# Optimization experiments

Hardware: AMD Instinct MI355X
Metric: run time of the kernel (lower is better)

The kernel has to match this reference:

```python
import jax, jax.numpy as jnp
import numpy as np

THETA = 10000.0

def apply_rope(x, positions):
    # x: [B, H, S, d_k], positions: [S] int
    d_k = x.shape[-1]
    inv_freq = THETA ** (-jnp.arange(0, d_k, 2, dtype=jnp.float32) / d_k)  # [d_k/2]
    ang = positions.astype(jnp.float32)[:, None] * inv_freq[None, :]        # [S, d_k/2]
    cos, sin = jnp.cos(ang), jnp.sin(ang)
    x_even = x[..., 0::2]
    x_odd = x[..., 1::2]
    r_even = x_even * cos - x_odd * sin
    r_odd = x_even * sin + x_odd * cos
    # interleave back
    return jnp.stack([r_even, r_odd], axis=-1).reshape(x.shape)

def setup_inputs() -> dict:
    key = jax.random.key(0)
    k1, k2, k3 = jax.random.split(key, 3)
    B, S, D = 2, 2048, 1024
    x = jax.random.normal(k1, (B, S, D), dtype=jnp.float32)
    token_positions = jnp.arange(S, dtype=jnp.int32)
    W_qkv = jax.random.normal(k2, (3 * D, D), dtype=jnp.float32) * 0.02
    W_o = jax.random.normal(k3, (D, D), dtype=jnp.float32) * 0.02
    return {"x": x, "token_positions": token_positions, "W_qkv": W_qkv, "W_o": W_o}

def reference(x, token_positions, W_qkv, W_o):
    B, S, D = x.shape
    H = 16
    d_k = D // H
    qkv = jnp.einsum('bsd,ed->bse', x, W_qkv)           # [B, S, 3D]
    q, k, v = jnp.split(qkv, 3, axis=-1)
    def to_heads(t):
        return t.reshape(B, S, H, d_k).transpose(0, 2, 1, 3)  # [B, H, S, d_k]
    hq, hk, hv = to_heads(q), to_heads(k), to_heads(v)
    hq = apply_rope(hq, token_positions)
    hk = apply_rope(hk, token_positions)
    scale = d_k ** -0.5
    scores = jnp.einsum('bhqd,bhkd->bhqk', hq, hk) * scale  # [B, H, S, S]
    causal = jnp.tril(jnp.ones((S, S), dtype=bool))
    scores = jnp.where(causal, scores, -jnp.inf)
    attn = jax.nn.softmax(scores, axis=-1)
    out = jnp.einsum('bhqk,bhkd->bhqd', attn, hv)           # [B, H, S, d_k]
    out = out.transpose(0, 2, 1, 3).reshape(B, S, D)
    return jnp.einsum('bsd,ed->bse', out, W_o)
```

## Files before the change

kernel.cpp:

```cpp
#include <hip/hip_runtime.h>
#include <math.h>

typedef short short8 __attribute__((ext_vector_type(8)));
typedef float f32x4 __attribute__((ext_vector_type(4)));
typedef unsigned int u32x2 __attribute__((ext_vector_type(2)));

typedef __attribute__((address_space(1))) const void* as1p;
typedef __attribute__((address_space(3))) void* as3p;

__device__ __forceinline__ unsigned short f2bf(float f) {
    unsigned int u = __float_as_uint(f);
    u += 0x7fffu + ((u >> 16) & 1u);
    return (unsigned short)(u >> 16);
}

__global__ void cvt_all_bf16(const float* __restrict__ x,
                             const float* __restrict__ wqkv,
                             const float* __restrict__ wo,
                             unsigned short* __restrict__ xb,
                             unsigned short* __restrict__ wqkvb,
                             unsigned short* __restrict__ wob) {
    int i = blockIdx.x * blockDim.x + threadIdx.x;
    const float* src;
    unsigned short* dst;
    int off;
    if (i < 1048576)       { src = x;    dst = xb;    off = i; }
    else if (i < 1835008)  { src = wqkv; dst = wqkvb; off = i - 1048576; }
    else                   { src = wo;   dst = wob;   off = i - 1835008; }
    float4 v = ((const float4*)src)[off];
    ushort4 o = make_ushort4(f2bf(v.x), f2bf(v.y), f2bf(v.z), f2bf(v.w));
    ((ushort4*)dst)[off] = o;
}

template <int RF, int NTX, bool BF16_OUT, bool DO_ROPE>
__global__ __launch_bounds__(256) void gemm_nt_mfma(
    const unsigned short* __restrict__ A, const unsigned short* __restrict__ B,
    void* __restrict__ Cv, const int* __restrict__ pos, int N, int K) {
    constexpr int BM = RF * 32;
    __shared__ unsigned short As[BM * 32];
    __shared__ unsigned short Bs[128 * 32];
    const int tid = threadIdx.x;
    const int wave = tid >> 6, lane = tid & 63;
    const int L = blockIdx.x;
    const int xcd = L & 7, idx = L >> 3;
    const int nt_ = xcd * NTX + idx % NTX;
    const int mt  = idx / NTX;
    const int m0 = mt * BM, n0 = nt_ << 7;
    const int wr = ((wave >> 1) & 1) * (RF * 16);
    const int wc = (wave & 1) << 6;

    const int r0 = tid >> 2;
    const int ko = (((tid & 3) ^ ((r0 >> 1) & 3)) << 3);
    const unsigned short* Ap0 = A + (size_t)(m0 + r0) * K + ko;
    const unsigned short* Ap1 = A + (size_t)(m0 + (RF == 4 ? 64 : 0) + r0) * K + ko;
    const unsigned short* Bp0 = B + (size_t)(n0 + r0) * K + ko;
    const unsigned short* Bp1 = B + (size_t)(n0 + 64 + r0) * K + ko;

    f32x4 acc[RF][4] = {};
    const int lro = lane & 15;
    const int cs = ((lane >> 4) ^ ((lro >> 1) & 3)) << 3;

    for (int k0 = 0; k0 < K; k0 += 32) {
        __syncthreads();
        __builtin_amdgcn_global_load_lds((as1p)(Ap0 + k0), (as3p)(As + tid * 8), 16, 0, 0);
        if constexpr (RF == 4)
            __builtin_amdgcn_global_load_lds((as1p)(Ap1 + k0), (as3p)(As + (256 + tid) * 8), 16, 0, 0);
        __builtin_amdgcn_global_load_lds((as1p)(Bp0 + k0), (as3p)(Bs + tid * 8), 16, 0, 0);
        __builtin_amdgcn_global_load_lds((as1p)(Bp1 + k0), (as3p)(Bs + (256 + tid) * 8), 16, 0, 0);
        __syncthreads();

        short8 af[RF], bfr[4];
        #pragma unroll
        for (int i = 0; i < RF; i++) af[i] = *(const short8*)&As[(wr + i * 16 + lro) * 32 + cs];
        #pragma unroll
        for (int j = 0; j < 4; j++) bfr[j] = *(const short8*)&Bs[(wc + j * 16 + lro) * 32 + cs];
        #pragma unroll
        for (int i = 0; i < RF; i++)
            #pragma unroll
            for (int j = 0; j < 4; j++)
                acc[i][j] = __builtin_amdgcn_mfma_f32_16x16x32_bf16(af[i], bfr[j], acc[i][j], 0, 0, 0);
    }

    const int row_b = m0 + wr + ((lane >> 4) << 2);
    const int col_b = n0 + wc + lro;

    if constexpr (DO_ROPE) {
        const int sec = (n0 + wc) >> 10;
        if (sec < 2) {
            const float qs = (sec == 0) ? 0.18033688011112042f : 1.0f;
            const float sgn = (lane & 1) ? 1.0f : -1.0f;
            float ps[RF * 4];
            #pragma unroll
            for (int i = 0; i < RF; i++)
                #pragma unroll
                for (int r = 0; r < 4; r++)
                    ps[i * 4 + r] = (float)pos[(row_b + i * 16 + r) & 2047];
            #pragma unroll
            for (int j = 0; j < 4; j++) {
                float invf_rev = exp2f(-(float)((lro >> 1) + 8 * j) * 0.41524101186092029f)
                                 * 0.15915494309189535f;
                #pragma unroll
                for (int i = 0; i < RF; i++)
                    #pragma unroll
                    for (int r = 0; r < 4; r++) {
                        float rev = ps[i * 4 + r] * invf_rev;
                        rev -= floorf(rev);
                        float c = __builtin_amdgcn_cosf(rev) * qs;
                        float s = __builtin_amdgcn_sinf(rev) * (qs * sgn);
                        float mine = acc[i][j][r];
                        float partner = __shfl_xor(mine, 1, 64);
                        acc[i][j][r] = mine * c + partner * s;
                    }
            }
        }
    }

    #pragma unroll
    for (int i = 0; i < RF; i++)
        #pragma unroll
        for (int j = 0; j < 4; j++)
            #pragma unroll
            for (int r = 0; r < 4; r++) {
                size_t idx2 = (size_t)(row_b + i * 16 + r) * N + (col_b + j * 16);
                if constexpr (BF16_OUT) ((unsigned short*)Cv)[idx2] = f2bf(acc[i][j][r]);
                else ((float*)Cv)[idx2] = acc[i][j][r];
            }
}

__global__ __launch_bounds__(256, 3) void flash_attn_mfma(
    const unsigned short* __restrict__ qkv, unsigned short* __restrict__ Ows) {
    const int S = 2048, D3 = 3072;
    const int L = blockIdx.x;
    const int xcd = L & 7, rr = L >> 3;
    const int qt = 31 - (rr >> 2);
    const int g2 = xcd + ((rr & 3) << 3);
    const int h = g2 & 15, b = g2 >> 4;
    const int tid = threadIdx.x, wave = tid >> 6, lane = tid & 63;
    const int lro = lane & 15, grp = lane >> 4;

    __shared__ __align__(16) unsigned int Vp[64 * 34];
    __shared__ float RedW[4][16][66];
    __shared__ float Lbuf[4][4][16];

    const int kp = lane >> 3;
    const int vo = (lane & 7) << 3;
    const int wcb = wave << 3;
    const int klb = (wave << 4) + (grp << 2);

    const unsigned short* kbg = qkv + (size_t)(b * S) * D3 + 1024 + h * 64;
    const unsigned short* vbg = qkv + (size_t)(b * S) * D3 + 2048 + h * 64;

    const int q0 = qt << 6;
    const int nkt = qt + 1;

    short8 bq[4][2];
    #pragma unroll
    for (int f = 0; f < 4; f++) {
        const unsigned short* qrow =
            qkv + (size_t)(b * S + q0 + f * 16 + lro) * D3 + h * 64 + grp * 8;
        bq[f][0] = *(const short8*)qrow;
        bq[f][1] = *(const short8*)(qrow + 32);
    }

    const unsigned short* kfp = kbg + (size_t)(16 * wave + lro) * D3 + grp * 8;
    const unsigned short* vfp = vbg + (size_t)(16 * wave + 2 * kp) * D3 + vo;

    short8 kc0 = *(const short8*)kfp;
    short8 kc1 = *(const short8*)(kfp + 32);
    {
        uint4 va = *(const uint4*)vfp;
        uint4 vb = *(const uint4*)(vfp + D3);
        const unsigned short* pa_ = (const unsigned short*)&va;
        const unsigned short* pb_ = (const unsigned short*)&vb;
        #pragma unroll
        for (int j = 0; j < 8; j++)
            Vp[(vo + j) * 34 + wcb + kp] = (unsigned)pa_[j] | ((unsigned)pb_[j] << 16);
    }

    f32x4 acc[4][4] = {};
    float lsum[4] = {0.f, 0.f, 0.f, 0.f};

    for (int kt = 0; kt < nkt; kt++) {
        const bool pf = (kt + 1 < nkt);
        short8 kn0, kn1;
        uint4 vna, vnb;
        if (pf) {
            const size_t off = (size_t)((kt + 1) * 64) * D3;
            kn0 = *(const short8*)(kfp + off);
            kn1 = *(const short8*)(kfp + off + 32);
            vna = *(const uint4*)(vfp + off);
            vnb = *(const uint4*)(vfp + off + D3);
        }

        f32x4 s0 = {}, s1 = {}, s2 = {}, s3 = {};
        s0 = __builtin_amdgcn_mfma_f32_16x16x32_bf16(kc0, bq[0][0], s0, 0, 0, 0);
        s0 = __builtin_amdgcn_mfma_f32_16x16x32_bf16(kc1, bq[0][1], s0, 0, 0, 0);
        s1 = __builtin_amdgcn_mfma_f32_16x16x32_bf16(kc0, bq[1][0], s1, 0, 0, 0);
        s1 = __builtin_amdgcn_mfma_f32_16x16x32_bf16(kc1, bq[1][1], s1, 0, 0, 0);
        s2 = __builtin_amdgcn_mfma_f32_16x16x32_bf16(kc0, bq[2][0], s2, 0, 0, 0);
        s2 = __builtin_amdgcn_mfma_f32_16x16x32_bf16(kc1, bq[2][1], s2, 0, 0, 0);
        s3 = __builtin_amdgcn_mfma_f32_16x16x32_bf16(kc0, bq[3][0], s3, 0, 0, 0);
        s3 = __builtin_amdgcn_mfma_f32_16x16x32_bf16(kc1, bq[3][1], s3, 0, 0, 0);
        f32x4 sf[4] = {s0, s1, s2, s3};

        const bool dg = (kt == nkt - 1);
        u32x2 pw[4];
        #pragma unroll
        for (int f = 0; f < 4; f++) {
            float v0 = sf[f][0], v1 = sf[f][1], v2 = sf[f][2], v3 = sf[f][3];
            if (dg) {
                int thr = (f << 4) + lro - klb;
                if (0 > thr) v0 = -1e30f;
                if (1 > thr) v1 = -1e30f;
                if (2 > thr) v2 = -1e30f;
                if (3 > thr) v3 = -1e30f;
            }
            float p0 = __builtin_amdgcn_exp2f(v0);
            float p1 = __builtin_amdgcn_exp2f(v1);
            float p2 = __builtin_amdgcn_exp2f(v2);
            float p3 = __builtin_amdgcn_exp2f(v3);
            lsum[f] += (p0 + p1) + (p2 + p3);
            unsigned u0, u1;
            asm("v_cvt_pk_bf16_f32 %0, %1, %2" : "=v"(u0) : "v"(p0), "v"(p1));
            asm("v_cvt_pk_bf16_f32 %0, %1, %2" : "=v"(u1) : "v"(p2), "v"(p3));
            pw[f][0] = u0;
            pw[f][1] = u1;
        }

        u32x2 vv[4];
        #pragma unroll
        for (int nt = 0; nt < 4; nt++)
            vv[nt] = *(const u32x2*)&Vp[(nt * 16 + lro) * 34 + wcb + (grp << 1)];

        #pragma unroll
        for (int f = 0; f < 4; f++)
            #pragma unroll
            for (int nt = 0; nt < 4; nt++)
                asm("v_mfma_f32_16x16x16_bf16 %0, %1, %2, %0"
                    : "+v"(acc[f][nt]) : "v"(pw[f]), "v"(vv[nt]));

        if (pf) {
            const unsigned short* pa_ = (const unsigned short*)&vna;
            const unsigned short* pb_ = (const unsigned short*)&vnb;
            #pragma unroll
            for (int j = 0; j < 8; j++)
                Vp[(vo + j) * 34 + wcb + kp] = (unsigned)pa_[j] | ((unsigned)pb_[j] << 16);
            kc0 = kn0;
            kc1 = kn1;
        }
    }

    #pragma unroll
    for (int f = 0; f < 4; f++) {
        lsum[f] += __shfl_xor(lsum[f], 16, 64);
        lsum[f] += __shfl_xor(lsum[f], 32, 64);
    }
    if (lane < 16) {
        #pragma unroll
        for (int f = 0; f < 4; f++) Lbuf[wave][f][lro] = lsum[f];
    }

    #pragma unroll
    for (int f = 0; f < 4; f++) {
        __syncthreads();
        if (wave != f) {
            #pragma unroll
            for (int nt = 0; nt < 4; nt++)
                #pragma unroll
                for (int r = 0; r < 4; r++)
                    RedW[wave][(grp << 2) + r][nt * 16 + lro] = acc[f][nt][r];
        }
        __syncthreads();
        if (wave == f) {
            #pragma unroll
            for (int w2 = 0; w2 < 4; w2++) {
                if (w2 == f) continue;
                #pragma unroll
                for (int nt = 0; nt < 4; nt++)
                    #pragma unroll
                    for (int r = 0; r < 4; r++)
                        acc[f][nt][r] += RedW[w2][(grp << 2) + r][nt * 16 + lro];
            }
            #pragma unroll
            for (int r = 0; r < 4; r++) {
                int q = (grp << 2) + r;
                float lt = Lbuf[0][f][q] + Lbuf[1][f][q] +
                           Lbuf[2][f][q] + Lbuf[3][f][q];
                float inv = 1.0f / lt;
                int row = q0 + (f << 4) + q;
                #pragma unroll
                for (int nt = 0; nt < 4; nt++)
                    Ows[(size_t)(b * S + row) * 1024 + h * 64 + nt * 16 + lro] =
                        f2bf(acc[f][nt][r] * inv);
            }
        }
    }
}

extern "C" void kernel_launch(void* const* d_in, const int* in_sizes, int n_in,
                              void* d_out, int out_size, void* d_ws, size_t ws_size,
                              hipStream_t stream) {
    const float* x    = (const float*)d_in[0];
    const int*   pos  = (const int*)d_in[1];
    const float* Wqkv = (const float*)d_in[2];
    const float* Wo   = (const float*)d_in[3];
    float* out = (float*)d_out;

    unsigned short* xb    = (unsigned short*)d_ws;
    unsigned short* Wqkvb = xb + (size_t)4096 * 1024;
    unsigned short* Wob   = Wqkvb + (size_t)3072 * 1024;
    unsigned short* qkvb  = Wob + (size_t)1024 * 1024;
    unsigned short* Owsb  = qkvb + (size_t)4096 * 3072;

    cvt_all_bf16<<<8192, 256, 0, stream>>>(x, Wqkv, Wo, xb, Wqkvb, Wob);

    gemm_nt_mfma<4, 3, true, true><<<768, 256, 0, stream>>>(
        xb, Wqkvb, qkvb, pos, 3072, 1024);

    flash_attn_mfma<<<1024, 256, 0, stream>>>(qkvb, Owsb);

    gemm_nt_mfma<2, 1, false, false><<<512, 256, 0, stream>>>(
        Owsb, Wob, out, nullptr, 1024, 1024);
}
```

Before: 196.0 us.

## Pair complementary causal query tiles per block and double-buffer V in LDS

Each attention block now handles two query tiles, qt and 31-qt, so every block does the same amount of causal work, and the grid shrinks to 512 blocks. The V staging in shared memory becomes double-buffered, with a 35-word padded stride and a cooperative block-wide load. A __syncthreads is added on every key-tile iteration. The aim is to remove load imbalance from causal tiles, at the cost of extra per-iteration barriers, fewer blocks in flight, and a dropped occupancy hint in launch_bounds.

```diff
diff --git a/kernel.cpp b/kernel.cpp
--- a/kernel.cpp
+++ b/kernel.cpp
@@ -127,171 +127,182 @@
             }
 }
 
-__global__ __launch_bounds__(256, 3) void flash_attn_mfma(
+__global__ __launch_bounds__(256) void flash_attn_mfma(
     const unsigned short* __restrict__ qkv, unsigned short* __restrict__ Ows) {
     const int S = 2048, D3 = 3072;
-    const int L = blockIdx.x;
-    const int xcd = L & 7, rr = L >> 3;
-    const int qt = 31 - (rr >> 2);
-    const int g2 = xcd + ((rr & 3) << 3);
+    const int L = blockIdx.x + (blockIdx.y << 4) + (blockIdx.z << 8);
+    const int xcd = L & 7, t = L >> 3;
+    const int pp = t & 15;
+    const int g2 = xcd + ((t >> 4) << 3);
     const int h = g2 & 15, b = g2 >> 4;
     const int tid = threadIdx.x, wave = tid >> 6, lane = tid & 63;
     const int lro = lane & 15, grp = lane >> 4;
 
-    __shared__ __align__(16) unsigned int Vp[64 * 34];
+    __shared__ __align__(16) unsigned int Vp[2][64 * 35];
     __shared__ float RedW[4][16][66];
     __shared__ float Lbuf[4][4][16];
 
-    const int kp = lane >> 3;
-    const int vo = (lane & 7) << 3;
-    const int wcb = wave << 3;
+    const int m = tid >> 3;
+    const int vo = (tid & 7) << 3;
+    const int vcb = (wave << 3) + (grp << 1);
     const int klb = (wave << 4) + (grp << 2);
 
     const unsigned short* kbg = qkv + (size_t)(b * S) * D3 + 1024 + h * 64;
     const unsigned short* vbg = qkv + (size_t)(b * S) * D3 + 2048 + h * 64;
 
-    const int q0 = qt << 6;
-    const int nkt = qt + 1;
-
-    short8 bq[4][2];
-    #pragma unroll
-    for (int f = 0; f < 4; f++) {
-        const unsigned short* qrow =
-            qkv + (size_t)(b * S + q0 + f * 16 + lro) * D3 + h * 64 + grp * 8;
-        bq[f][0] = *(const short8*)qrow;
-        bq[f][1] = *(const short8*)(qrow + 32);
-    }
-
     const unsigned short* kfp = kbg + (size_t)(16 * wave + lro) * D3 + grp * 8;
-    const unsigned short* vfp = vbg + (size_t)(16 * wave + 2 * kp) * D3 + vo;
-
-    short8 kc0 = *(const short8*)kfp;
-    short8 kc1 = *(const short8*)(kfp + 32);
-    {
-        uint4 va = *(const uint4*)vfp;
-        uint4 vb = *(const uint4*)(vfp + D3);
-        const unsigned short* pa_ = (const unsigned short*)&va;
-        const unsigned short* pb_ = (const unsigned short*)&vb;
-        #pragma unroll
-        for (int j = 0; j < 8; j++)
-            Vp[(vo + j) * 34 + wcb + kp] = (unsigned)pa_[j] | ((unsigned)pb_[j] << 16);
-    }
-
-    f32x4 acc[4][4] = {};
-    float lsum[4] = {0.f, 0.f, 0.f, 0.f};
-
-    for (int kt = 0; kt < nkt; kt++) {
-        const bool pf = (kt + 1 < nkt);
-        short8 kn0, kn1;
-        uint4 vna, vnb;
-        if (pf) {
-            const size_t off = (size_t)((kt + 1) * 64) * D3;
-            kn0 = *(const short8*)(kfp + off);
-            kn1 = *(const short8*)(kfp + off + 32);
-            vna = *(const uint4*)(vfp + off);
-            vnb = *(const uint4*)(vfp + off + D3);
-        }
-
-        f32x4 s0 = {}, s1 = {}, s2 = {}, s3 = {};
-        s0 = __builtin_amdgcn_mfma_f32_16x16x32_bf16(kc0, bq[0][0], s0, 0, 0, 0);
-        s0 = __builtin_amdgcn_mfma_f32_16x16x32_bf16(kc1, bq[0][1], s0, 0, 0, 0);
-        s1 = __builtin_amdgcn_mfma_f32_16x16x32_bf16(kc0, bq[1][0], s1, 0, 0, 0);
-        s1 = __builtin_amdgcn_mfma_f32_16x16x32_bf16(kc1, bq[1][1], s1, 0, 0, 0);
-        s2 = __builtin_amdgcn_mfma_f32_16x16x32_bf16(kc0, bq[2][0], s2, 0, 0, 0);
-        s2 = __builtin_amdgcn_mfma_f32_16x16x32_bf16(kc1, bq[2][1], s2, 0, 0, 0);
-        s3 = __builtin_amdgcn_mfma_f32_16x16x32_bf16(kc0, bq[3][0], s3, 0, 0, 0);
-        s3 = __builtin_amdgcn_mfma_f32_16x16x32_bf16(kc1, bq[3][1], s3, 0, 0, 0);
-        f32x4 sf[4] = {s0, s1, s2, s3};
-
-        const bool dg = (kt == nkt - 1);
-        u32x2 pw[4];
+    const unsigned short* vfp = vbg + (size_t)(2 * m) * D3 + vo;
+
+    for (int ph = 0; ph < 2; ph++) {
+        const int qt = ph ? 31 - pp : pp;
+        const int q0 = qt << 6;
+        const int nkt = qt + 1;
+
+        __syncthreads();
+
+        short8 bq[4][2];
         #pragma unroll
         for (int f = 0; f < 4; f++) {
-            float v0 = sf[f][0], v1 = sf[f][1], v2 = sf[f][2], v3 = sf[f][3];
-            if (dg) {
-                int thr = (f << 4) + lro - klb;
-                if (0 > thr) v0 = -1e30f;
-                if (1 > thr) v1 = -1e30f;
-                if (2 > thr) v2 = -1e30f;
-                if (3 > thr) v3 = -1e30f;
-            }
-            float p0 = __builtin_amdgcn_exp2f(v0);
-            float p1 = __builtin_amdgcn_exp2f(v1);
-            float p2 = __builtin_amdgcn_exp2f(v2);
-            float p3 = __builtin_amdgcn_exp2f(v3);
-            lsum[f] += (p0 + p1) + (p2 + p3);
-            unsigned u0, u1;
-            asm("v_cvt_pk_bf16_f32 %0, %1, %2" : "=v"(u0) : "v"(p0), "v"(p1));
-            asm("v_cvt_pk_bf16_f32 %0, %1, %2" : "=v"(u1) : "v"(p2), "v"(p3));
-            pw[f][0] = u0;
-            pw[f][1] = u1;
-        }
-
-        u32x2 vv[4];
-        #pragma unroll
-        for (int nt = 0; nt < 4; nt++)
-            vv[nt] = *(const u32x2*)&Vp[(nt * 16 + lro) * 34 + wcb + (grp << 1)];
-
-        #pragma unroll
-        for (int f = 0; f < 4; f++)
-            #pragma unroll
-            for (int nt = 0; nt < 4; nt++)
-                asm("v_mfma_f32_16x16x16_bf16 %0, %1, %2, %0"
-                    : "+v"(acc[f][nt]) : "v"(pw[f]), "v"(vv[nt]));
-
-        if (pf) {
-            const unsigned short* pa_ = (const unsigned short*)&vna;
-            const unsigned short* pb_ = (const unsigned short*)&vnb;
+            const unsigned short* qrow =
+                qkv + (size_t)(b * S + q0 + f * 16 + lro) * D3 + h * 64 + grp * 8;
+            bq[f][0] = *(const short8*)qrow;
+            bq[f][1] = *(const short8*)(qrow + 32);
+        }
+
+        short8 kc0 = *(const short8*)kfp;
+        short8 kc1 = *(const short8*)(kfp + 32);
+        {
+            uint4 va = *(const uint4*)vfp;
+            uint4 vb = *(const uint4*)(vfp + D3);
+            const unsigned short* pa_ = (const unsigned short*)&va;
+            const unsigned short* pb_ = (const unsigned short*)&vb;
             #pragma unroll
             for (int j = 0; j < 8; j++)
-                Vp[(vo + j) * 34 + wcb + kp] = (unsigned)pa_[j] | ((unsigned)pb_[j] << 16);
-            kc0 = kn0;
-            kc1 = kn1;
-        }
-    }
-
-    #pragma unroll
-    for (int f = 0; f < 4; f++) {
-        lsum[f] += __shfl_xor(lsum[f], 16, 64);
-        lsum[f] += __shfl_xor(lsum[f], 32, 64);
-    }
-    if (lane < 16) {
-        #pragma unroll
-        for (int f = 0; f < 4; f++) Lbuf[wave][f][lro] = lsum[f];
-    }
-
-    #pragma unroll
-    for (int f = 0; f < 4; f++) {
+                Vp[0][(vo + j) * 35 + m] = (unsigned)pa_[j] | ((unsigned)pb_[j] << 16);
+        }
         __syncthreads();
-        if (wave != f) {
-            #pragma unroll
-            for (int nt = 0; nt < 4; nt++)
-                #pragma unroll
-                for (int r = 0; r < 4; r++)
-                    RedW[wave][(grp << 2) + r][nt * 16 + lro] = acc[f][nt][r];
-        }
-        __syncthreads();
-        if (wave == f) {
-            #pragma unroll
-            for (int w2 = 0; w2 < 4; w2++) {
-                if (w2 == f) continue;
+
+        f32x4 acc[4][4] = {};
+        float lsum[4] = {0.f, 0.f, 0.f, 0.f};
+
+        for (int kt = 0; kt < nkt; kt++) {
+            const int cur = kt & 1, nxt = cur ^ 1;
+            const bool pf = (kt + 1 < nkt);
+            short8 kn0, kn1;
+            uint4 vna, vnb;
+            if (pf) {
+                const size_t off = (size_t)((kt + 1) * 64) * D3;
+                kn0 = *(const short8*)(kfp + off);
+                kn1 = *(const short8*)(kfp + off + 32);
+                vna = *(const uint4*)(vfp + off);
+                vnb = *(const uint4*)(vfp + off + D3);
+            }
+
+            f32x4 s0 = {}, s1 = {}, s2 = {}, s3 = {};
+            s0 = __builtin_amdgcn_mfma_f32_16x16x32_bf16(kc0, bq[0][0], s0, 0, 0, 0);
+            s0 = __builtin_amdgcn_mfma_f32_16x16x32_bf16(kc1, bq[0][1], s0, 0, 0, 0);
+            s1 = __builtin_amdgcn_mfma_f32_16x16x32_bf16(kc0, bq[1][0], s1, 0, 0, 0);
+            s1 = __builtin_amdgcn_mfma_f32_16x16x32_bf16(kc1, bq[1][1], s1, 0, 0, 0);
+            s2 = __builtin_amdgcn_mfma_f32_16x16x32_bf16(kc0, bq[2][0], s2, 0, 0, 0);
+            s2 = __builtin_amdgcn_mfma_f32_16x16x32_bf16(kc1, bq[2][1], s2, 0, 0, 0);
+            s3 = __builtin_amdgcn_mfma_f32_16x16x32_bf16(kc0, bq[3][0], s3, 0, 0, 0);
+            s3 = __builtin_amdgcn_mfma_f32_16x16x32_bf16(kc1, bq[3][1], s3, 0, 0, 0);
+            f32x4 sf[4] = {s0, s1, s2, s3};
+
+            const bool dg = (kt == nkt - 1);
+            u32x2 pw[4];
+            #pragma unroll
+            for (int f = 0; f < 4; f++) {
+                float v0 = sf[f][0], v1 = sf[f][1], v2 = sf[f][2], v3 = sf[f][3];
+                if (dg) {
+                    int thr = (f << 4) + lro - klb;
+                    if (0 > thr) v0 = -1e30f;
+                    if (1 > thr) v1 = -1e30f;
+                    if (2 > thr) v2 = -1e30f;
+                    if (3 > thr) v3 = -1e30f;
+                }
+                float p0 = __builtin_amdgcn_exp2f(v0);
+                float p1 = __builtin_amdgcn_exp2f(v1);
+                float p2 = __builtin_amdgcn_exp2f(v2);
+                float p3 = __builtin_amdgcn_exp2f(v3);
+                lsum[f] += (p0 + p1) + (p2 + p3);
+                unsigned u0, u1;
+                asm("v_cvt_pk_bf16_f32 %0, %1, %2" : "=v"(u0) : "v"(p0), "v"(p1));
+                asm("v_cvt_pk_bf16_f32 %0, %1, %2" : "=v"(u1) : "v"(p2), "v"(p3));
+                pw[f][0] = u0;
+                pw[f][1] = u1;
+            }
+
+            u32x2 vv[4];
+            #pragma unroll
+            for (int nt = 0; nt < 4; nt++) {
+                const unsigned* vr = &Vp[cur][(nt * 16 + lro) * 35 + vcb];
+                vv[nt][0] = vr[0];
+                vv[nt][1] = vr[1];
+            }
+
+            #pragma unroll
+            for (int f = 0; f < 4; f++)
+                #pragma unroll
+                for (int nt = 0; nt < 4; nt++)
+                    asm("v_mfma_f32_16x16x16_bf16 %0, %1, %2, %0"
+                        : "+v"(acc[f][nt]) : "v"(pw[f]), "v"(vv[nt]));
+
+            if (pf) {
+                const unsigned short* pa_ = (const unsigned short*)&vna;
+                const unsigned short* pb_ = (const unsigned short*)&vnb;
+                #pragma unroll
+                for (int j = 0; j < 8; j++)
+                    Vp[nxt][(vo + j) * 35 + m] = (unsigned)pa_[j] | ((unsigned)pb_[j] << 16);
+                kc0 = kn0;
+                kc1 = kn1;
+            }
+            __syncthreads();
+        }
+
+        #pragma unroll
+        for (int f = 0; f < 4; f++) {
+            lsum[f] += __shfl_xor(lsum[f], 16, 64);
+            lsum[f] += __shfl_xor(lsum[f], 32, 64);
+        }
+        if (lane < 16) {
+            #pragma unroll
+            for (int f = 0; f < 4; f++) Lbuf[wave][f][lro] = lsum[f];
+        }
+
+        #pragma unroll
+        for (int f = 0; f < 4; f++) {
+            __syncthreads();
+            if (wave != f) {
                 #pragma unroll
                 for (int nt = 0; nt < 4; nt++)
                     #pragma unroll
                     for (int r = 0; r < 4; r++)
-                        acc[f][nt][r] += RedW[w2][(grp << 2) + r][nt * 16 + lro];
-            }
-            #pragma unroll
-            for (int r = 0; r < 4; r++) {
-                int q = (grp << 2) + r;
-                float lt = Lbuf[0][f][q] + Lbuf[1][f][q] +
-                           Lbuf[2][f][q] + Lbuf[3][f][q];
-                float inv = 1.0f / lt;
-                int row = q0 + (f << 4) + q;
-                #pragma unroll
-                for (int nt = 0; nt < 4; nt++)
-                    Ows[(size_t)(b * S + row) * 1024 + h * 64 + nt * 16 + lro] =
-                        f2bf(acc[f][nt][r] * inv);
+                        RedW[wave][(grp << 2) + r][nt * 16 + lro] = acc[f][nt][r];
+            }
+            __syncthreads();
+            if (wave == f) {
+                #pragma unroll
+                for (int w2 = 0; w2 < 4; w2++) {
+                    if (w2 == f) continue;
+                    #pragma unroll
+                    for (int nt = 0; nt < 4; nt++)
+                        #pragma unroll
+                        for (int r = 0; r < 4; r++)
+                            acc[f][nt][r] += RedW[w2][(grp << 2) + r][nt * 16 + lro];
+                }
+                #pragma unroll
+                for (int r = 0; r < 4; r++) {
+                    int q = (grp << 2) + r;
+                    float lt = Lbuf[0][f][q] + Lbuf[1][f][q] +
+                               Lbuf[2][f][q] + Lbuf[3][f][q];
+                    float inv = 1.0f / lt;
+                    int row = q0 + (f << 4) + q;
+                    #pragma unroll
+                    for (int nt = 0; nt < 4; nt++)
+                        Ows[(size_t)(b * S + row) * 1024 + h * 64 + nt * 16 + lro] =
+                            f2bf(acc[f][nt][r] * inv);
+                }
             }
         }
     }
@@ -317,7 +328,7 @@
     gemm_nt_mfma<4, 3, true, true><<<768, 256, 0, stream>>>(
         xb, Wqkvb, qkvb, pos, 3072, 1024);
 
-    flash_attn_mfma<<<1024, 256, 0, stream>>>(qkvb, Owsb);
+    flash_attn_mfma<<<dim3(16, 16, 2), 256, 0, stream>>>(qkvb, Owsb);
 
     gemm_nt_mfma<2, 1, false, false><<<512, 256, 0, stream>>>(
         Owsb, Wob, out, nullptr, 1024, 1024);
```

Measured after the change: 180.2 us (median of 2 runs). 1.09x faster.
